# Kernel tuning notes

Hardware: AMD Instinct MI355X
Metric: run time of the kernel (lower is better)

The kernel has to match this reference:

```python
import jax, jax.numpy as jnp
import numpy as np

EMB = 384
HEAD_DIM = 64  # emb_size / num_head = 384 / 6
B, S = 8, 2048


def setup_inputs() -> dict:
    key = jax.random.key(0)
    k1, k2, k3, k4 = jax.random.split(key, 4)
    x = jax.random.normal(k1, (B, S, EMB), dtype=jnp.float32)
    # nn.Linear(emb, head_dim, bias=False): store as [in, out] so q = x @ W
    scale = 0.02
    Wq = jax.random.normal(k2, (EMB, HEAD_DIM), dtype=jnp.float32) * scale
    Wk = jax.random.normal(k3, (EMB, HEAD_DIM), dtype=jnp.float32) * scale
    Wv = jax.random.normal(k4, (EMB, HEAD_DIM), dtype=jnp.float32) * scale
    return {"x": x, "Wq": Wq, "Wk": Wk, "Wv": Wv}


def reference(x, Wq, Wk, Wv):
    # x: [B, S, C]
    q = jnp.einsum('bsc,cd->bsd', x, Wq)  # [B,S,D]
    k = jnp.einsum('bsc,cd->bsd', x, Wk)
    v = jnp.einsum('bsc,cd->bsd', x, Wv)
    scores = jnp.einsum('bid,bjd->bij', q, k) * (HEAD_DIM ** -0.5)  # [B,S,S]
    # causal mask: positions with tril==0 (j > i) set to -inf
    causal = jnp.tril(jnp.ones((S, S), dtype=bool))  # [S,S]
    scores = jnp.where(causal[None, :, :], scores, -jnp.inf)
    # NOTE: faithful to original — softmax over dim=1 (query axis), not -1.
    attn = jax.nn.softmax(scores, axis=1)  # [B,S,S]
    out = jnp.einsum('bij,bjd->bid', attn, v)  # [B,S,D]
    return out
```

## Files before the change

### kernel.cpp

```cpp
#include <hip/hip_runtime.h>
#include <hip/hip_bf16.h>
#include <math.h>

#define B_N 8
#define S_N 2048
#define C_N 384
#define D_N 64
#define NEG_BIG (-1e30f)

typedef __bf16 bf16x8 __attribute__((ext_vector_type(8)));
typedef float f32x4 __attribute__((ext_vector_type(4)));

static __device__ __forceinline__ bf16x8 ldfrag(const __bf16* p) {
  return *reinterpret_cast<const bf16x8*>(p);
}

static __device__ __forceinline__ void gload16(void* lds, const void* gsrc) {
  __builtin_amdgcn_global_load_lds(
      (const __attribute__((address_space(1))) unsigned int*)gsrc,
      (__attribute__((address_space(3))) unsigned int*)lds, 16, 0, 0);
}

__global__ __launch_bounds__(256) void w_prep(
    const float* __restrict__ Wq, const float* __restrict__ Wk,
    const float* __restrict__ Wv, __bf16* __restrict__ Wt) {
  const int idx = blockIdx.x * 256 + threadIdx.x;
  const int m = idx / (64 * C_N);
  const int r = idx % (64 * C_N);
  const int d = r / C_N;
  const int c = r % C_N;
  const float* W = (m == 0) ? Wq : (m == 1) ? Wk : Wv;
  Wt[idx] = (__bf16)W[c * 64 + d];
}

__global__ __launch_bounds__(384) void qkv_mfma(
    const float* __restrict__ x, const __bf16* __restrict__ Wt,
    __bf16* __restrict__ Q, __bf16* __restrict__ K, __bf16* __restrict__ Vt) {
  const int t = threadIdx.x;
  const int w = t >> 6, lane = t & 63, lr = lane & 15, lg = lane >> 4;
  const int mat = w >> 1, rh = w & 1;
  const int row0 = blockIdx.x * 32;
  const int ri = row0 + rh * 16 + lr;

  __shared__ __bf16 vtile[32][66];

  const float scl = (mat == 0) ? 0.125f : 1.0f;
  const float* xr = x + (size_t)ri * C_N;
  const __bf16* Wm = Wt + (size_t)mat * 64 * C_N;

  f32x4 acc[4];
#pragma unroll
  for (int nt = 0; nt < 4; ++nt) acc[nt] = {0.f, 0.f, 0.f, 0.f};

#pragma unroll 4
  for (int kk = 0; kk < C_N / 32; ++kk) {
    const float4 xa = *reinterpret_cast<const float4*>(xr + kk * 32 + lg * 8);
    const float4 xb = *reinterpret_cast<const float4*>(xr + kk * 32 + lg * 8 + 4);
    bf16x8 a;
    a[0] = (__bf16)(xa.x * scl); a[1] = (__bf16)(xa.y * scl);
    a[2] = (__bf16)(xa.z * scl); a[3] = (__bf16)(xa.w * scl);
    a[4] = (__bf16)(xb.x * scl); a[5] = (__bf16)(xb.y * scl);
    a[6] = (__bf16)(xb.z * scl); a[7] = (__bf16)(xb.w * scl);
#pragma unroll
    for (int nt = 0; nt < 4; ++nt) {
      const bf16x8 bw = ldfrag(Wm + (size_t)(nt * 16 + lr) * C_N + kk * 32 + lg * 8);
      acc[nt] = __builtin_amdgcn_mfma_f32_16x16x32_bf16(a, bw, acc[nt], 0, 0, 0);
    }
  }

  if (mat < 2) {
    __bf16* outp = (mat == 0) ? Q : K;
#pragma unroll
    for (int nt = 0; nt < 4; ++nt)
#pragma unroll
      for (int r = 0; r < 4; ++r)
        outp[(size_t)(row0 + rh * 16 + lg * 4 + r) * 64 + nt * 16 + lr] =
            (__bf16)acc[nt][r];
  } else {
#pragma unroll
    for (int nt = 0; nt < 4; ++nt)
#pragma unroll
      for (int r = 0; r < 4; ++r)
        vtile[rh * 16 + lg * 4 + r][nt * 16 + lr] = (__bf16)acc[nt][r];
  }
  __syncthreads();

  const int b = row0 >> 11, s0 = row0 & (S_N - 1);
  for (int idx = t; idx < 64 * 32; idx += 384) {
    const int d = idx >> 5, s2 = idx & 31;
    Vt[((size_t)b * D_N + d) * S_N + s0 + s2] = vtile[s2][d];
  }
}

__global__ __launch_bounds__(1024) void col_stats(
    const __bf16* __restrict__ Q, const __bf16* __restrict__ K,
    float* __restrict__ rZ) {
  const int wg = blockIdx.x;
  const int b  = wg & 7;
  const int jb = wg >> 3;
  const int j0 = jb * 64;

  const int t = threadIdx.x;
  const int w = t >> 6;
  const int s = w & 3;
  const int q = w >> 2;
  const int lane = t & 63, lr = lane & 15, lg = lane >> 4;

  __shared__ __align__(16) __bf16 QT[2][64][64];
  __shared__ float zs[4][4][16];

  const __bf16* Qb = Q + (size_t)b * S_N * 64;
  const __bf16* Kb = K + (size_t)b * S_N * 64;

  const int krow = j0 + q * 16 + lr;
  const bf16x8 bk0 = ldfrag(Kb + (size_t)krow * 64 + lg * 8);
  const bf16x8 bk1 = ldfrag(Kb + (size_t)krow * 64 + 32 + lg * 8);

  const int str  = t & 511;
  const int srow = str >> 3;
  const int schk = str & 7;
  const int gchk = schk ^ (srow & 7);
  const bool stager = (t < 512);

  if (stager)
    gload16(&QT[0][srow][schk * 8], Qb + (size_t)(j0 + srow) * 64 + gchk * 8);
  __syncthreads();

  float z = 0.f;
  int cur = 0;
  for (int it = jb; it < 32; ++it) {
    const int i0 = it * 64;
    if (it + 1 < 32 && stager)
      gload16(&QT[cur ^ 1][srow][schk * 8],
              Qb + (size_t)(i0 + 64 + srow) * 64 + gchk * 8);

    const int arow = s * 16 + lr;
    const bf16x8 aq0 = ldfrag(&QT[cur][arow][(lg ^ (arow & 7)) * 8]);
    const bf16x8 aq1 = ldfrag(&QT[cur][arow][((4 + lg) ^ (arow & 7)) * 8]);

    f32x4 s4 = {0.f, 0.f, 0.f, 0.f};
    s4 = __builtin_amdgcn_mfma_f32_16x16x32_bf16(aq0, bk0, s4, 0, 0, 0);
    s4 = __builtin_amdgcn_mfma_f32_16x16x32_bf16(aq1, bk1, s4, 0, 0, 0);

    const int ibase = i0 + s * 16 + lg * 4;
    const int jg = j0 + q * 16 + lr;
    if (it == jb) {
#pragma unroll
      for (int r = 0; r < 4; ++r)
        if (ibase + r < jg) s4[r] = NEG_BIG;
    }
    float es = __expf(s4[0]) + __expf(s4[1]) + __expf(s4[2]) + __expf(s4[3]);
    es += __shfl_xor(es, 16);
    es += __shfl_xor(es, 32);
    z += es;

    __syncthreads();
    cur ^= 1;
  }

  if (lg == 0) zs[s][q][lr] = z;
  __syncthreads();
  if (s == 0 && lg == 0) {
    const float zt = zs[0][q][lr] + zs[1][q][lr] + zs[2][q][lr] + zs[3][q][lr];
    rZ[(size_t)b * S_N + j0 + q * 16 + lr] = 1.0f / zt;
  }
}

__global__ __launch_bounds__(1024) void attn_out(
    const __bf16* __restrict__ Q, const __bf16* __restrict__ K,
    const __bf16* __restrict__ Vt, const float* __restrict__ rZ,
    float* __restrict__ out) {
  const int wg = blockIdx.x;
  const int b  = wg & 7;
  const int ib = wg >> 3;

  const int t = threadIdx.x;
  const int w = t >> 6;
  const int s = w & 3;
  const int q = w >> 2;
  const int lane = t & 63, lr = lane & 15, lg = lane >> 4;
  const int i0 = ib * 64;

  __shared__ __align__(16) __bf16 KT[2][64][64];
  __shared__ __align__(16) __bf16 VT[2][64][64];
  __shared__ __align__(16) __bf16 P[4][16][72];

  const __bf16* Qb  = Q  + (size_t)b * S_N * 64;
  const __bf16* Kb  = K  + (size_t)b * S_N * 64;
  const __bf16* Vtb = Vt + (size_t)b * D_N * S_N;
  const float*  rZb = rZ + (size_t)b * S_N;

  const int str  = t & 511;
  const int srow = str >> 3;
  const int schk = str & 7;
  const int gchk = schk ^ (srow & 7);
  const bool isK = (t < 512);

  const int ri = i0 + s * 16 + lr;
  const bf16x8 aq0 = ldfrag(Qb + (size_t)ri * 64 + lg * 8);
  const bf16x8 aq1 = ldfrag(Qb + (size_t)ri * 64 + 32 + lg * 8);
  const int ibase = i0 + s * 16 + lg * 4;

  f32x4 o = {0.f, 0.f, 0.f, 0.f};

  if (isK) gload16(&KT[0][srow][schk * 8], Kb + (size_t)srow * 64 + gchk * 8);
  else     gload16(&VT[0][srow][schk * 8], Vtb + (size_t)srow * S_N + gchk * 8);
  __syncthreads();

  int cur = 0;
  for (int jb = 0; jb <= ib; ++jb) {
    const int j0 = jb * 64;
    if (jb + 1 <= ib) {
      const int j0n = j0 + 64;
      if (isK) gload16(&KT[cur ^ 1][srow][schk * 8],
                       Kb + (size_t)(j0n + srow) * 64 + gchk * 8);
      else     gload16(&VT[cur ^ 1][srow][schk * 8],
                       Vtb + (size_t)srow * S_N + j0n + gchk * 8);
    }

    const int krow = q * 16 + lr;
    const bf16x8 bk0 = ldfrag(&KT[cur][krow][(lg ^ (krow & 7)) * 8]);
    const bf16x8 bk1 = ldfrag(&KT[cur][krow][((4 + lg) ^ (krow & 7)) * 8]);
    f32x4 s4 = {0.f, 0.f, 0.f, 0.f};
    s4 = __builtin_amdgcn_mfma_f32_16x16x32_bf16(aq0, bk0, s4, 0, 0, 0);
    s4 = __builtin_amdgcn_mfma_f32_16x16x32_bf16(aq1, bk1, s4, 0, 0, 0);

    const int jg = j0 + q * 16 + lr;
    const float rz = rZb[jg];
#pragma unroll
    for (int r = 0; r < 4; ++r) {
      const float pv = (jg <= ibase + r) ? __expf(s4[r]) * rz : 0.f;
      P[s][lg * 4 + r][q * 16 + lr] = (__bf16)pv;
    }
    __syncthreads();

    const bf16x8 ap0 = ldfrag(&P[s][lr][lg * 8]);
    const bf16x8 ap1 = ldfrag(&P[s][lr][32 + lg * 8]);
    const int vrow = q * 16 + lr;
    const bf16x8 bv0 = ldfrag(&VT[cur][vrow][(lg ^ (vrow & 7)) * 8]);
    const bf16x8 bv1 = ldfrag(&VT[cur][vrow][((4 + lg) ^ (vrow & 7)) * 8]);
    o = __builtin_amdgcn_mfma_f32_16x16x32_bf16(ap0, bv0, o, 0, 0, 0);
    o = __builtin_amdgcn_mfma_f32_16x16x32_bf16(ap1, bv1, o, 0, 0, 0);
    __syncthreads();
    cur ^= 1;
  }

  float* ob = out + (size_t)b * S_N * D_N;
#pragma unroll
  for (int r = 0; r < 4; ++r)
    ob[(size_t)(i0 + s * 16 + lg * 4 + r) * 64 + q * 16 + lr] = o[r];
}

extern "C" void kernel_launch(void* const* d_in, const int* in_sizes, int n_in,
                              void* d_out, int out_size, void* d_ws, size_t ws_size,
                              hipStream_t stream) {
  (void)in_sizes; (void)n_in; (void)ws_size; (void)out_size;
  const float* x  = (const float*)d_in[0];
  const float* Wq = (const float*)d_in[1];
  const float* Wk = (const float*)d_in[2];
  const float* Wv = (const float*)d_in[3];
  float* out = (float*)d_out;

  __bf16* Qb = (__bf16*)d_ws;
  __bf16* Kb = Qb + (size_t)B_N * S_N * D_N;
  __bf16* Vt = Kb + (size_t)B_N * S_N * D_N;
  float* rZ = (float*)(Vt + (size_t)B_N * S_N * D_N);
  __bf16* Wt = (__bf16*)(rZ + (size_t)B_N * S_N);

  w_prep<<<dim3(3 * 64 * C_N / 256), dim3(256), 0, stream>>>(Wq, Wk, Wv, Wt);
  qkv_mfma<<<dim3(B_N * S_N / 32), dim3(384), 0, stream>>>(x, Wt, Qb, Kb, Vt);
  col_stats<<<dim3(32 * B_N), dim3(1024), 0, stream>>>(Qb, Kb, rZ);
  attn_out<<<dim3(32 * B_N), dim3(1024), 0, stream>>>(Qb, Kb, Vt, rZ, out);
}
```

Before: 83.03 us.

## Split col_stats and attn_out work in halves across blocks, add combine kernel

The column-statistics and attention-output kernels now launch twice as many blocks, each handling half of the causal iteration range, and write partial sums. A new combine kernel adds the two output partials, and attn_out computes the reciprocal normalizer from the two z partials. This targets load imbalance and low occupancy from only 256 blocks with triangular work, at the cost of an extra launch and extra fp32 partial traffic. The QKV projection loop also gains software prefetching of the next x and W fragments into registers.

```diff
diff --git a/kernel.cpp b/kernel.cpp
--- a/kernel.cpp
+++ b/kernel.cpp
@@ -52,20 +52,34 @@
 #pragma unroll
   for (int nt = 0; nt < 4; ++nt) acc[nt] = {0.f, 0.f, 0.f, 0.f};
 
-#pragma unroll 4
+  float4 xa = *reinterpret_cast<const float4*>(xr + lg * 8);
+  float4 xb = *reinterpret_cast<const float4*>(xr + lg * 8 + 4);
+  bf16x8 bw[4];
+#pragma unroll
+  for (int nt = 0; nt < 4; ++nt)
+    bw[nt] = ldfrag(Wm + (size_t)(nt * 16 + lr) * C_N + lg * 8);
+
   for (int kk = 0; kk < C_N / 32; ++kk) {
-    const float4 xa = *reinterpret_cast<const float4*>(xr + kk * 32 + lg * 8);
-    const float4 xb = *reinterpret_cast<const float4*>(xr + kk * 32 + lg * 8 + 4);
+    const int kn = (kk + 1 < C_N / 32) ? kk + 1 : kk;
+    const float4 xan = *reinterpret_cast<const float4*>(xr + kn * 32 + lg * 8);
+    const float4 xbn = *reinterpret_cast<const float4*>(xr + kn * 32 + lg * 8 + 4);
+    bf16x8 bwn[4];
+#pragma unroll
+    for (int nt = 0; nt < 4; ++nt)
+      bwn[nt] = ldfrag(Wm + (size_t)(nt * 16 + lr) * C_N + kn * 32 + lg * 8);
+
     bf16x8 a;
     a[0] = (__bf16)(xa.x * scl); a[1] = (__bf16)(xa.y * scl);
     a[2] = (__bf16)(xa.z * scl); a[3] = (__bf16)(xa.w * scl);
     a[4] = (__bf16)(xb.x * scl); a[5] = (__bf16)(xb.y * scl);
     a[6] = (__bf16)(xb.z * scl); a[7] = (__bf16)(xb.w * scl);
 #pragma unroll
-    for (int nt = 0; nt < 4; ++nt) {
-      const bf16x8 bw = ldfrag(Wm + (size_t)(nt * 16 + lr) * C_N + kk * 32 + lg * 8);
-      acc[nt] = __builtin_amdgcn_mfma_f32_16x16x32_bf16(a, bw, acc[nt], 0, 0, 0);
-    }
+    for (int nt = 0; nt < 4; ++nt)
+      acc[nt] = __builtin_amdgcn_mfma_f32_16x16x32_bf16(a, bw[nt], acc[nt], 0, 0, 0);
+
+    xa = xan; xb = xbn;
+#pragma unroll
+    for (int nt = 0; nt < 4; ++nt) bw[nt] = bwn[nt];
   }
 
   if (mat < 2) {
@@ -94,10 +108,11 @@
 
 __global__ __launch_bounds__(1024) void col_stats(
     const __bf16* __restrict__ Q, const __bf16* __restrict__ K,
-    float* __restrict__ rZ) {
+    float* __restrict__ zpart) {
   const int wg = blockIdx.x;
   const int b  = wg & 7;
-  const int jb = wg >> 3;
+  const int jb = (wg >> 3) & 31;
+  const int h  = wg >> 8;
   const int j0 = jb * 64;
 
   const int t = threadIdx.x;
@@ -106,8 +121,20 @@
   const int q = w >> 2;
   const int lane = t & 63, lr = lane & 15, lg = lane >> 4;
 
+  const int n = 32 - jb;
+  const int itStart = (h == 0) ? jb : jb + (n + 1) / 2;
+  const int itEnd   = (h == 0) ? jb + (n + 1) / 2 : 32;
+  float* zout = zpart + (size_t)h * B_N * S_N + (size_t)b * S_N;
+
   __shared__ __align__(16) __bf16 QT[2][64][64];
   __shared__ float zs[4][4][16];
+
+  if (itStart >= itEnd) {
+    if (w == 0 && lg == 0) {
+      for (int c = lr; c < 64; c += 16) zout[j0 + c] = 0.f;
+    }
+    return;
+  }
 
   const __bf16* Qb = Q + (size_t)b * S_N * 64;
   const __bf16* Kb = K + (size_t)b * S_N * 64;
@@ -123,14 +150,15 @@
   const bool stager = (t < 512);
 
   if (stager)
-    gload16(&QT[0][srow][schk * 8], Qb + (size_t)(j0 + srow) * 64 + gchk * 8);
+    gload16(&QT[0][srow][schk * 8],
+            Qb + (size_t)(itStart * 64 + srow) * 64 + gchk * 8);
   __syncthreads();
 
   float z = 0.f;
   int cur = 0;
-  for (int it = jb; it < 32; ++it) {
+  for (int it = itStart; it < itEnd; ++it) {
     const int i0 = it * 64;
-    if (it + 1 < 32 && stager)
+    if (it + 1 < itEnd && stager)
       gload16(&QT[cur ^ 1][srow][schk * 8],
               Qb + (size_t)(i0 + 64 + srow) * 64 + gchk * 8);
 
@@ -162,17 +190,18 @@
   __syncthreads();
   if (s == 0 && lg == 0) {
     const float zt = zs[0][q][lr] + zs[1][q][lr] + zs[2][q][lr] + zs[3][q][lr];
-    rZ[(size_t)b * S_N + j0 + q * 16 + lr] = 1.0f / zt;
+    zout[j0 + q * 16 + lr] = zt;
   }
 }
 
 __global__ __launch_bounds__(1024) void attn_out(
     const __bf16* __restrict__ Q, const __bf16* __restrict__ K,
-    const __bf16* __restrict__ Vt, const float* __restrict__ rZ,
-    float* __restrict__ out) {
+    const __bf16* __restrict__ Vt, const float* __restrict__ zpart,
+    float* __restrict__ opart) {
   const int wg = blockIdx.x;
   const int b  = wg & 7;
-  const int ib = wg >> 3;
+  const int ib = (wg >> 3) & 31;
+  const int h  = wg >> 8;
 
   const int t = threadIdx.x;
   const int w = t >> 6;
@@ -181,6 +210,19 @@
   const int lane = t & 63, lr = lane & 15, lg = lane >> 4;
   const int i0 = ib * 64;
 
+  const int n = ib + 1;
+  const int jbStart = (h == 0) ? 0 : (n + 1) / 2;
+  const int jbEnd   = (h == 0) ? (n + 1) / 2 : n;
+
+  float* op = opart + (size_t)h * B_N * S_N * D_N + (size_t)b * S_N * D_N;
+
+  if (jbStart >= jbEnd) {
+#pragma unroll
+    for (int r = 0; r < 4; ++r)
+      op[(size_t)(i0 + s * 16 + lg * 4 + r) * 64 + q * 16 + lr] = 0.f;
+    return;
+  }
+
   __shared__ __align__(16) __bf16 KT[2][64][64];
   __shared__ __align__(16) __bf16 VT[2][64][64];
   __shared__ __align__(16) __bf16 P[4][16][72];
@@ -188,7 +230,8 @@
   const __bf16* Qb  = Q  + (size_t)b * S_N * 64;
   const __bf16* Kb  = K  + (size_t)b * S_N * 64;
   const __bf16* Vtb = Vt + (size_t)b * D_N * S_N;
-  const float*  rZb = rZ + (size_t)b * S_N;
+  const float*  zp0 = zpart + (size_t)b * S_N;
+  const float*  zp1 = zpart + (size_t)B_N * S_N + (size_t)b * S_N;
 
   const int str  = t & 511;
   const int srow = str >> 3;
@@ -203,14 +246,16 @@
 
   f32x4 o = {0.f, 0.f, 0.f, 0.f};
 
-  if (isK) gload16(&KT[0][srow][schk * 8], Kb + (size_t)srow * 64 + gchk * 8);
-  else     gload16(&VT[0][srow][schk * 8], Vtb + (size_t)srow * S_N + gchk * 8);
+  if (isK) gload16(&KT[0][srow][schk * 8],
+                   Kb + (size_t)(jbStart * 64 + srow) * 64 + gchk * 8);
+  else     gload16(&VT[0][srow][schk * 8],
+                   Vtb + (size_t)srow * S_N + jbStart * 64 + gchk * 8);
   __syncthreads();
 
   int cur = 0;
-  for (int jb = 0; jb <= ib; ++jb) {
+  for (int jb = jbStart; jb < jbEnd; ++jb) {
     const int j0 = jb * 64;
-    if (jb + 1 <= ib) {
+    if (jb + 1 < jbEnd) {
       const int j0n = j0 + 64;
       if (isK) gload16(&KT[cur ^ 1][srow][schk * 8],
                        Kb + (size_t)(j0n + srow) * 64 + gchk * 8);
@@ -226,7 +271,7 @@
     s4 = __builtin_amdgcn_mfma_f32_16x16x32_bf16(aq1, bk1, s4, 0, 0, 0);
 
     const int jg = j0 + q * 16 + lr;
-    const float rz = rZb[jg];
+    const float rz = 1.0f / (zp0[jg] + zp1[jg]);
 #pragma unroll
     for (int r = 0; r < 4; ++r) {
       const float pv = (jg <= ibase + r) ? __expf(s4[r]) * rz : 0.f;
@@ -245,10 +290,15 @@
     cur ^= 1;
   }
 
-  float* ob = out + (size_t)b * S_N * D_N;
 #pragma unroll
   for (int r = 0; r < 4; ++r)
-    ob[(size_t)(i0 + s * 16 + lg * 4 + r) * 64 + q * 16 + lr] = o[r];
+    op[(size_t)(i0 + s * 16 + lg * 4 + r) * 64 + q * 16 + lr] = o[r];
+}
+
+__global__ __launch_bounds__(256) void combine(
+    const float* __restrict__ opart, float* __restrict__ out) {
+  const size_t idx = (size_t)blockIdx.x * 256 + threadIdx.x;
+  out[idx] = opart[idx] + opart[(size_t)B_N * S_N * D_N + idx];
 }
 
 extern "C" void kernel_launch(void* const* d_in, const int* in_sizes, int n_in,
@@ -264,11 +314,13 @@
   __bf16* Qb = (__bf16*)d_ws;
   __bf16* Kb = Qb + (size_t)B_N * S_N * D_N;
   __bf16* Vt = Kb + (size_t)B_N * S_N * D_N;
-  float* rZ = (float*)(Vt + (size_t)B_N * S_N * D_N);
-  __bf16* Wt = (__bf16*)(rZ + (size_t)B_N * S_N);
+  float* zpart = (float*)(Vt + (size_t)B_N * S_N * D_N);
+  float* opart = zpart + (size_t)2 * B_N * S_N;
+  __bf16* Wt = (__bf16*)(opart + (size_t)2 * B_N * S_N * D_N);
 
   w_prep<<<dim3(3 * 64 * C_N / 256), dim3(256), 0, stream>>>(Wq, Wk, Wv, Wt);
   qkv_mfma<<<dim3(B_N * S_N / 32), dim3(384), 0, stream>>>(x, Wt, Qb, Kb, Vt);
-  col_stats<<<dim3(32 * B_N), dim3(1024), 0, stream>>>(Qb, Kb, rZ);
-  attn_out<<<dim3(32 * B_N), dim3(1024), 0, stream>>>(Qb, Kb, Vt, rZ, out);
-}
+  col_stats<<<dim3(2 * 32 * B_N), dim3(1024), 0, stream>>>(Qb, Kb, zpart);
+  attn_out<<<dim3(2 * 32 * B_N), dim3(1024), 0, stream>>>(Qb, Kb, Vt, zpart, opart);
+  combine<<<dim3(B_N * S_N * D_N / 256), dim3(256), 0, stream>>>(opart, out);
+}
```

Result: faster. 76.96 us (-7.3%).
